# Performance work log

Measured on AMD Instinct MI355X. Metric: run time of the kernel, lower is better.

Reference implementation:

```python
import jax, jax.numpy as jnp
import numpy as np

N_HEAD, D_MODEL, D_K, D_V = 16, 1024, 64, 64
B, L = 8, 1024
LN_EPS = 1e-5
NEG_INF = -1e9


def setup_inputs() -> dict:
    key = jax.random.key(0)
    ks = jax.random.split(key, 12)
    s = 0.02
    return {
        "q": jax.random.normal(ks[0], (B, L, D_MODEL), jnp.float32),
        "k": jax.random.normal(ks[1], (B, L, D_MODEL), jnp.float32),
        "v": jax.random.normal(ks[2], (B, L, D_MODEL), jnp.float32),
        "mask": jnp.zeros((B, L, L), dtype=bool),
        "wq": jax.random.normal(ks[3], (D_MODEL, N_HEAD * D_K), jnp.float32) * s,
        "bq": jnp.zeros((N_HEAD * D_K,), jnp.float32),
        "wk": jax.random.normal(ks[4], (D_MODEL, N_HEAD * D_K), jnp.float32) * s,
        "bk": jnp.zeros((N_HEAD * D_K,), jnp.float32),
        "wv": jax.random.normal(ks[5], (D_MODEL, N_HEAD * D_V), jnp.float32) * s,
        "bv": jnp.zeros((N_HEAD * D_V,), jnp.float32),
        "wo": jax.random.normal(ks[6], (N_HEAD * D_V, D_MODEL), jnp.float32) * s,
        "bo": jnp.zeros((D_MODEL,), jnp.float32),
        "gamma": jnp.ones((D_MODEL,), jnp.float32),
        "beta": jnp.zeros((D_MODEL,), jnp.float32),
    }


def reference(q, k, v, mask, wq, bq, wk, bk, wv, bv, wo, bo, gamma, beta):
    b, lq, _ = q.shape
    lk = k.shape[1]
    residual = q
    # separate Q/K/V projections, split heads: [b, len, h, d]
    qh = (q @ wq + bq).reshape(b, lq, N_HEAD, D_K)
    kh = (k @ wk + bk).reshape(b, lk, N_HEAD, D_K)
    vh = (v @ wv + bv).reshape(b, lk, N_HEAD, D_V)
    # scaled dot-product attention (temperature = sqrt(d_k))
    scores = jnp.einsum("bqhd,bkhd->bhqk", qh, kh) / jnp.sqrt(jnp.float32(D_K))
    scores = jnp.where(mask[:, None, :, :], NEG_INF, scores)
    attn = jax.nn.softmax(scores, axis=-1)  # [b, h, lq, lk]
    ctx = jnp.einsum("bhqk,bkhd->bqhd", attn, vh).reshape(b, lq, N_HEAD * D_V)
    # out-proj (dropout is identity in eval) + residual + LayerNorm
    out = ctx @ wo + bo + residual
    mu = out.mean(-1, keepdims=True)
    var = out.var(-1, keepdims=True)
    out = (out - mu) * jax.lax.rsqrt(var + LN_EPS) * gamma + beta
    # match original attn layout: [n_head*b, lq, lk]
    attn_flat = attn.transpose(1, 0, 2, 3).reshape(N_HEAD * b, lq, lk)
    return out, attn_flat
```

## Files before the change

kernel.cpp:

```cpp
#include <hip/hip_runtime.h>
#include <stdint.h>

static constexpr int BATCH  = 8;
static constexpr int SEQ    = 1024;
static constexpr int DMODEL = 1024;
static constexpr int NHEAD  = 16;

typedef __attribute__((ext_vector_type(8))) short sh8;
typedef __attribute__((ext_vector_type(4))) float fl4;

__device__ __forceinline__ uint16_t f2bf(float f) {
    union { float f; uint32_t u; } a; a.f = f;
    uint32_t r = a.u + 0x7FFFu + ((a.u >> 16) & 1u);
    return (uint16_t)(r >> 16);
}

__device__ __forceinline__ float b2f(uint16_t u) {
    union { uint32_t u; float f; } a; a.u = ((uint32_t)u) << 16; return a.f;
}

__device__ __forceinline__ sh8 pack_bf8(fl4 x0, fl4 x1) {
    union { uint16_t u[8]; sh8 v; } pk;
    pk.u[0] = f2bf(x0[0]); pk.u[1] = f2bf(x0[1]); pk.u[2] = f2bf(x0[2]); pk.u[3] = f2bf(x0[3]);
    pk.u[4] = f2bf(x1[0]); pk.u[5] = f2bf(x1[1]); pk.u[6] = f2bf(x1[2]); pk.u[7] = f2bf(x1[3]);
    return pk.v;
}

__device__ __forceinline__ fl4 mfma16(sh8 a, sh8 b, fl4 c) {
    return __builtin_amdgcn_mfma_f32_16x16x32_bf16(a, b, c, 0, 0, 0);
}

__device__ __forceinline__ void gload16(const void* g, void* l) {
    __builtin_amdgcn_global_load_lds(
        (const __attribute__((address_space(1))) void*)g,
        (__attribute__((address_space(3))) void*)l, 16, 0, 0);
}

__global__ __launch_bounds__(256) void cvt_bf16_kernel(const float* __restrict__ src,
                                                       uint16_t* __restrict__ dst) {
    const int t = blockIdx.x * 256 + threadIdx.x;
    #pragma unroll
    for (int it = 0; it < 2; ++it) {
        const int i = (it * 524288 + t) * 8;
        fl4 x0 = *(const fl4*)(src + i), x1 = *(const fl4*)(src + i + 4);
        *(sh8*)(dst + i) = pack_bf8(x0, x1);
    }
}

__global__ __launch_bounds__(256) void wtrans_kernel(const float* __restrict__ w,
                                                     uint16_t* __restrict__ wT) {
    __shared__ uint16_t T[64][72];
    const int n0 = blockIdx.x * 64, k0 = blockIdx.y * 64;
    const int tid = threadIdx.x;
    #pragma unroll
    for (int it = 0; it < 4; ++it) {
        int g = it * 256 + tid;
        int r = g >> 4, c = (g & 15) * 4;
        fl4 x = *(const fl4*)(w + (size_t)(k0 + r) * DMODEL + n0 + c);
        T[r][c + 0] = f2bf(x[0]); T[r][c + 1] = f2bf(x[1]);
        T[r][c + 2] = f2bf(x[2]); T[r][c + 3] = f2bf(x[3]);
    }
    __syncthreads();
    #pragma unroll
    for (int it = 0; it < 4; ++it) {
        int g = it * 256 + tid;
        int r = g >> 4, c = (g & 15) * 4;
        ushort4 o;
        o.x = T[c + 0][r]; o.y = T[c + 1][r]; o.z = T[c + 2][r]; o.w = T[c + 3][r];
        *(ushort4*)(wT + (size_t)(n0 + r) * DMODEL + k0 + c) = o;
    }
}

__global__ __launch_bounds__(256) void vtrans_kernel(const uint16_t* __restrict__ vh,
                                                     uint16_t* __restrict__ vT) {
    __shared__ uint16_t T[64][72];
    const int l0 = blockIdx.x * 64, hd0 = blockIdx.y * 64, bb = blockIdx.z;
    const uint16_t* src = vh + (size_t)bb * SEQ * DMODEL;
    uint16_t* dst = vT + (size_t)bb * SEQ * DMODEL;
    const int tid = threadIdx.x;
    #pragma unroll
    for (int it = 0; it < 4; ++it) {
        int g = it * 256 + tid;
        int r = g >> 4, c = (g & 15) * 4;
        ushort4 x = *(const ushort4*)(src + (size_t)(l0 + r) * DMODEL + hd0 + c);
        T[r][c + 0] = x.x; T[r][c + 1] = x.y; T[r][c + 2] = x.z; T[r][c + 3] = x.w;
    }
    __syncthreads();
    #pragma unroll
    for (int it = 0; it < 4; ++it) {
        int g = it * 256 + tid;
        int r = g >> 4, c = (g & 15) * 4;
        ushort4 o;
        o.x = T[c + 0][r]; o.y = T[c + 1][r]; o.z = T[c + 2][r]; o.w = T[c + 3][r];
        *(ushort4*)(dst + (size_t)(hd0 + r) * DMODEL + l0 + c) = o;
    }
}

template<bool OUT_BF16, bool RESID>
__global__ __launch_bounds__(256)
void gemm128(const uint16_t* __restrict__ Ab, const uint16_t* __restrict__ Bt,
             const float* __restrict__ bias, const float* __restrict__ resid,
             void* __restrict__ Cv) {
    __shared__ uint16_t Alds[128 * 64];
    __shared__ uint16_t Blds[128 * 64];
    const int tid = threadIdx.x;
    const int m0 = blockIdx.y * 128, n0 = blockIdx.x * 128;
    const int lane = tid & 63, wid = tid >> 6;
    const int wr = (wid >> 1) * 64, wc = (wid & 1) * 64;
    const int fr = lane & 15, fk = (lane >> 4) * 8;

    fl4 acc[4][4];
    #pragma unroll
    for (int i = 0; i < 4; ++i)
        #pragma unroll
        for (int j = 0; j < 4; ++j) acc[i][j] = (fl4){0.f, 0.f, 0.f, 0.f};

    for (int kt = 0; kt < 16; ++kt) {
        const int kb = kt * 64;
        #pragma unroll
        for (int it = 0; it < 4; ++it) {
            const int g = it * 256 + tid;
            const int r = g >> 3, c = (g & 7) << 3;
            const int lofs = __builtin_amdgcn_readfirstlane((it * 256 + wid * 64) * 16);
            gload16(Ab + (size_t)(m0 + r) * DMODEL + kb + c, (char*)Alds + lofs);
            gload16(Bt + (size_t)(n0 + r) * DMODEL + kb + c, (char*)Blds + lofs);
        }
        __syncthreads();
        #pragma unroll
        for (int ks = 0; ks < 2; ++ks) {
            sh8 a[4], bb[4];
            #pragma unroll
            for (int mi = 0; mi < 4; ++mi) a[mi] = *(const sh8*)&Alds[(wr + mi * 16 + fr) * 64 + ks * 32 + fk];
            #pragma unroll
            for (int ni = 0; ni < 4; ++ni) bb[ni] = *(const sh8*)&Blds[(wc + ni * 16 + fr) * 64 + ks * 32 + fk];
            #pragma unroll
            for (int mi = 0; mi < 4; ++mi)
                #pragma unroll
                for (int ni = 0; ni < 4; ++ni) acc[mi][ni] = mfma16(a[mi], bb[ni], acc[mi][ni]);
        }
        __syncthreads();
    }

    #pragma unroll
    for (int mi = 0; mi < 4; ++mi) {
        #pragma unroll
        for (int ni = 0; ni < 4; ++ni) {
            const int col = n0 + wc + ni * 16 + fr;
            const float bv = bias[col];
            #pragma unroll
            for (int i = 0; i < 4; ++i) {
                const int row = m0 + wr + mi * 16 + (lane >> 4) * 4 + i;
                float val = acc[mi][ni][i] + bv;
                if (RESID) val += resid[(size_t)row * DMODEL + col];
                if (OUT_BF16) ((uint16_t*)Cv)[(size_t)row * DMODEL + col] = f2bf(val);
                else          ((float*)Cv)[(size_t)row * DMODEL + col] = val;
            }
        }
    }
}

__global__ __launch_bounds__(256)
void attn_kernel(const uint16_t* __restrict__ qh, const uint16_t* __restrict__ kh,
                 const uint16_t* __restrict__ vT, const uint8_t* __restrict__ mask,
                 float* __restrict__ attn, uint16_t* __restrict__ ctx) {
    __shared__ uint16_t S[16 * 1024];
    __shared__ float rinv[16];
    const int q0 = blockIdx.x * 16, h = blockIdx.y, b = blockIdx.z;
    const int tid = threadIdx.x, lane = tid & 63, wid = tid >> 6;
    const int fr = lane & 15, fk = (lane >> 4) * 8, frow4 = (lane >> 4) * 4;

    sh8 Aq[2];
    #pragma unroll
    for (int ks = 0; ks < 2; ++ks)
        Aq[ks] = *(const sh8*)(qh + (size_t)(b * SEQ + q0 + fr) * DMODEL + h * 64 + ks * 32 + fk);

    for (int t8 = 0; t8 < 8; ++t8) {
        const int kv0 = (t8 * 4 + wid) * 32;
        sh8 Bk[2][2];
        #pragma unroll
        for (int ni = 0; ni < 2; ++ni)
            #pragma unroll
            for (int ks = 0; ks < 2; ++ks)
                Bk[ni][ks] = *(const sh8*)(kh + (size_t)(b * SEQ + kv0 + ni * 16 + fr) * DMODEL + h * 64 + ks * 32 + fk);
        fl4 sa[2];
        #pragma unroll
        for (int ni = 0; ni < 2; ++ni) sa[ni] = (fl4){0.f, 0.f, 0.f, 0.f};
        #pragma unroll
        for (int ni = 0; ni < 2; ++ni)
            #pragma unroll
            for (int ks = 0; ks < 2; ++ks) sa[ni] = mfma16(Aq[ks], Bk[ni][ks], sa[ni]);
        #pragma unroll
        for (int ni = 0; ni < 2; ++ni)
            #pragma unroll
            for (int i = 0; i < 4; ++i) {
                const int row = frow4 + i, col = kv0 + ni * 16 + fr;
                S[row * 1024 + ((((col >> 3) ^ (row & 15)) << 3) | (col & 7))] = f2bf(sa[ni][i] * 0.125f);
            }
    }
    __syncthreads();

    {
        const int r = tid >> 4, j = tid & 15;
        const int rbase = r * 1024;
        const int rx = r & 15;
        const uint8_t* mbase = mask + (size_t)(b * SEQ + q0 + r) * SEQ;
        float mx = -1e30f;
        #pragma unroll
        for (int c4 = 0; c4 < 8; ++c4) {
            const int cc = c4 * 16 + j;
            const int so = rbase + ((cc ^ rx) << 3);
            sh8 sv = *(sh8*)&S[so];
            const uint2 mw = *(const uint2*)(mbase + cc * 8);
            union { uint16_t u[8]; sh8 v; } o;
            #pragma unroll
            for (int t = 0; t < 4; ++t) {
                float f = b2f((uint16_t)sv[t]);
                if ((mw.x >> (t * 8)) & 0xFF) f = -1e9f;
                o.u[t] = f2bf(f);
                mx = fmaxf(mx, f);
            }
            #pragma unroll
            for (int t = 0; t < 4; ++t) {
                float f = b2f((uint16_t)sv[4 + t]);
                if ((mw.y >> (t * 8)) & 0xFF) f = -1e9f;
                o.u[4 + t] = f2bf(f);
                mx = fmaxf(mx, f);
            }
            *(sh8*)&S[so] = o.v;
        }
        #pragma unroll
        for (int d = 1; d < 16; d <<= 1) mx = fmaxf(mx, __shfl_xor(mx, d));
        float sum = 0.f;
        #pragma unroll
        for (int c4 = 0; c4 < 8; ++c4) {
            const int cc = c4 * 16 + j;
            const int so = rbase + ((cc ^ rx) << 3);
            sh8 sv = *(sh8*)&S[so];
            union { uint16_t u[8]; sh8 v; } o;
            #pragma unroll
            for (int t = 0; t < 8; ++t) {
                float e = __expf(b2f((uint16_t)sv[t]) - mx);
                o.u[t] = f2bf(e);
                sum += e;
            }
            *(sh8*)&S[so] = o.v;
        }
        #pragma unroll
        for (int d = 1; d < 16; d <<= 1) sum += __shfl_xor(sum, d);
        if (j == 0) rinv[r] = 1.f / sum;
    }
    __syncthreads();

    {
        float* ab = attn + ((size_t)((h * BATCH + b) * SEQ + q0)) * SEQ;
        #pragma unroll
        for (int it = 0; it < 8; ++it) {
            const int gch = it * 256 + tid;
            const int row = gch >> 7, cc = gch & 127;
            sh8 p = *(sh8*)&S[row * 1024 + ((cc ^ (row & 15)) << 3)];
            const float ri = rinv[row];
            fl4 o0, o1;
            #pragma unroll
            for (int t = 0; t < 4; ++t) o0[t] = b2f((uint16_t)p[t]) * ri;
            #pragma unroll
            for (int t = 0; t < 4; ++t) o1[t] = b2f((uint16_t)p[4 + t]) * ri;
            float* dst = ab + (size_t)gch * 8;
            __builtin_nontemporal_store(o0, (fl4*)dst);
            __builtin_nontemporal_store(o1, (fl4*)(dst + 4));
        }
    }

    fl4 acc0 = (fl4){0.f, 0.f, 0.f, 0.f}, acc1 = (fl4){0.f, 0.f, 0.f, 0.f};
    const uint16_t* vbase = vT + (size_t)((b * NHEAD + h) * 64 + wid * 16) * SEQ;
    const int frx = fr & 15;
    #pragma unroll 4
    for (int ks2 = 0; ks2 < 32; ++ks2) {
        const int kv = ks2 * 32;
        sh8 Ap = *(const sh8*)&S[fr * 1024 + ((((kv + fk) >> 3) ^ frx) << 3)];
        sh8 Bv = *(const sh8*)(vbase + (size_t)fr * SEQ + kv + fk);
        if (ks2 & 1) acc1 = mfma16(Ap, Bv, acc1);
        else         acc0 = mfma16(Ap, Bv, acc0);
    }
    #pragma unroll
    for (int i = 0; i < 4; ++i) {
        const int q = frow4 + i;
        const float val = (acc0[i] + acc1[i]) * rinv[q];
        ctx[(size_t)(b * SEQ + q0 + q) * DMODEL + h * 64 + wid * 16 + fr] = f2bf(val);
    }
}

__global__ __launch_bounds__(256)
void ln_kernel(const float* __restrict__ raw, const float* __restrict__ gamma,
               const float* __restrict__ beta, float* __restrict__ out) {
    const int row = blockIdx.x;
    const int tid = threadIdx.x;
    const float* x = raw + (size_t)row * DMODEL;
    fl4 xv = *(const fl4*)(x + tid * 4);
    float s  = xv[0] + xv[1] + xv[2] + xv[3];
    float ss = xv[0] * xv[0] + xv[1] * xv[1] + xv[2] * xv[2] + xv[3] * xv[3];
    #pragma unroll
    for (int d = 1; d < 64; d <<= 1) { s += __shfl_xor(s, d); ss += __shfl_xor(ss, d); }
    __shared__ float sb[4], ssb[4];
    if ((tid & 63) == 0) { sb[tid >> 6] = s; ssb[tid >> 6] = ss; }
    __syncthreads();
    s  = sb[0] + sb[1] + sb[2] + sb[3];
    ss = ssb[0] + ssb[1] + ssb[2] + ssb[3];
    const float mu  = s * (1.f / 1024.f);
    const float var = ss * (1.f / 1024.f) - mu * mu;
    const float rstd = rsqrtf(var + 1e-5f);
    fl4 g  = *(const fl4*)(gamma + tid * 4);
    fl4 be = *(const fl4*)(beta + tid * 4);
    fl4 o;
    #pragma unroll
    for (int j = 0; j < 4; ++j) o[j] = (xv[j] - mu) * rstd * g[j] + be[j];
    *(fl4*)(out + (size_t)row * DMODEL + tid * 4) = o;
}

extern "C" void kernel_launch(void* const* d_in, const int* in_sizes, int n_in,
                              void* d_out, int out_size, void* d_ws, size_t ws_size,
                              hipStream_t stream) {
    (void)in_sizes; (void)n_in; (void)out_size; (void)ws_size;
    const float* q     = (const float*)d_in[0];
    const float* k     = (const float*)d_in[1];
    const float* v     = (const float*)d_in[2];
    const uint8_t* mask = (const uint8_t*)d_in[3];
    const float* wq = (const float*)d_in[4];
    const float* bq = (const float*)d_in[5];
    const float* wk = (const float*)d_in[6];
    const float* bk = (const float*)d_in[7];
    const float* wv = (const float*)d_in[8];
    const float* bv = (const float*)d_in[9];
    const float* wo = (const float*)d_in[10];
    const float* bo = (const float*)d_in[11];
    const float* gamma = (const float*)d_in[12];
    const float* beta  = (const float*)d_in[13];

    float* out  = (float*)d_out;
    float* attn = out + (size_t)BATCH * SEQ * DMODEL;

    uint16_t* qcvt = (uint16_t*)(attn);
    uint16_t* kcvt = (uint16_t*)((char*)attn + ((size_t)16 << 20));
    uint16_t* vcvt = (uint16_t*)((char*)attn + ((size_t)32 << 20));

    char* ws = (char*)d_ws;
    uint16_t* qh   = (uint16_t*)(ws);
    uint16_t* kh   = (uint16_t*)(ws + ((size_t)16 << 20));
    uint16_t* vT   = (uint16_t*)(ws + ((size_t)32 << 20));
    uint16_t* ctx  = (uint16_t*)(ws + ((size_t)48 << 20));
    uint16_t* wqT  = (uint16_t*)(ws + ((size_t)64 << 20));
    uint16_t* wkT  = (uint16_t*)(ws + ((size_t)66 << 20));
    uint16_t* wvT  = (uint16_t*)(ws + ((size_t)68 << 20));
    uint16_t* woT  = (uint16_t*)(ws + ((size_t)70 << 20));
    uint16_t* vtmp = (uint16_t*)(ws + ((size_t)72 << 20));

    dim3 tb(256);
    wtrans_kernel<<<dim3(16, 16), tb, 0, stream>>>(wq, wqT);
    wtrans_kernel<<<dim3(16, 16), tb, 0, stream>>>(wk, wkT);
    wtrans_kernel<<<dim3(16, 16), tb, 0, stream>>>(wv, wvT);
    wtrans_kernel<<<dim3(16, 16), tb, 0, stream>>>(wo, woT);

    cvt_bf16_kernel<<<2048, tb, 0, stream>>>(q, qcvt);
    cvt_bf16_kernel<<<2048, tb, 0, stream>>>(k, kcvt);
    cvt_bf16_kernel<<<2048, tb, 0, stream>>>(v, vcvt);

    gemm128<true, false><<<dim3(8, 64), tb, 0, stream>>>(qcvt, wqT, bq, nullptr, qh);
    gemm128<true, false><<<dim3(8, 64), tb, 0, stream>>>(kcvt, wkT, bk, nullptr, kh);
    gemm128<true, false><<<dim3(8, 64), tb, 0, stream>>>(vcvt, wvT, bv, nullptr, vtmp);

    vtrans_kernel<<<dim3(16, 16, 8), tb, 0, stream>>>(vtmp, vT);

    attn_kernel<<<dim3(64, NHEAD, BATCH), tb, 0, stream>>>(qh, kh, vT, mask, attn, ctx);

    gemm128<false, true><<<dim3(8, 64), tb, 0, stream>>>(ctx, woT, bo, q, out);

    ln_kernel<<<BATCH * SEQ, tb, 0, stream>>>(out, gamma, beta, out);
}
```

Baseline: 484.2 us.

## Batch weight transposes, conversions and QKV GEMMs; keep softmax row in registers

The four weight transposes, three fp32->bf16 conversions and three projection GEMMs are each merged into a single launch indexed by blockIdx.z. This cuts launch count and lets the three projection GEMMs fill the GPU together (1536 blocks instead of 512 per launch). The softmax now holds each thread's slice of the score row in registers, so it no longer re-reads shared memory between the max and exp passes. It also writes the fp32 attention output straight from registers instead of doing a separate synchronized pass over shared memory, at the cost of higher register pressure in the attention kernel.

```diff
diff --git a/kernel.cpp b/kernel.cpp
--- a/kernel.cpp
+++ b/kernel.cpp
@@ -36,8 +36,15 @@
         (__attribute__((address_space(3))) void*)l, 16, 0, 0);
 }
 
-__global__ __launch_bounds__(256) void cvt_bf16_kernel(const float* __restrict__ src,
-                                                       uint16_t* __restrict__ dst) {
+__global__ __launch_bounds__(256) void cvt3_kernel(const float* __restrict__ q,
+                                                   const float* __restrict__ k,
+                                                   const float* __restrict__ v,
+                                                   uint16_t* __restrict__ dq,
+                                                   uint16_t* __restrict__ dk,
+                                                   uint16_t* __restrict__ dv) {
+    const int z = blockIdx.z;
+    const float* src = (z == 0) ? q : (z == 1) ? k : v;
+    uint16_t* dst = (z == 0) ? dq : (z == 1) ? dk : dv;
     const int t = blockIdx.x * 256 + threadIdx.x;
     #pragma unroll
     for (int it = 0; it < 2; ++it) {
@@ -47,9 +54,14 @@
     }
 }
 
-__global__ __launch_bounds__(256) void wtrans_kernel(const float* __restrict__ w,
-                                                     uint16_t* __restrict__ wT) {
+__global__ __launch_bounds__(256) void wtrans_kernel(const float* __restrict__ wq, const float* __restrict__ wk,
+                                                     const float* __restrict__ wv, const float* __restrict__ wo,
+                                                     uint16_t* __restrict__ tq, uint16_t* __restrict__ tk,
+                                                     uint16_t* __restrict__ tv, uint16_t* __restrict__ to) {
     __shared__ uint16_t T[64][72];
+    const int z = blockIdx.z;
+    const float* w = (z == 0) ? wq : (z == 1) ? wk : (z == 2) ? wv : wo;
+    uint16_t* wT = (z == 0) ? tq : (z == 1) ? tk : (z == 2) ? tv : to;
     const int n0 = blockIdx.x * 64, k0 = blockIdx.y * 64;
     const int tid = threadIdx.x;
     #pragma unroll
@@ -97,14 +109,12 @@
 }
 
 template<bool OUT_BF16, bool RESID>
-__global__ __launch_bounds__(256)
-void gemm128(const uint16_t* __restrict__ Ab, const uint16_t* __restrict__ Bt,
-             const float* __restrict__ bias, const float* __restrict__ resid,
-             void* __restrict__ Cv) {
-    __shared__ uint16_t Alds[128 * 64];
-    __shared__ uint16_t Blds[128 * 64];
+__device__ __forceinline__
+void gemm_body(const uint16_t* __restrict__ Ab, const uint16_t* __restrict__ Bt,
+               const float* __restrict__ bias, const float* __restrict__ resid,
+               void* __restrict__ Cv, int m0, int n0,
+               uint16_t* Alds, uint16_t* Blds) {
     const int tid = threadIdx.x;
-    const int m0 = blockIdx.y * 128, n0 = blockIdx.x * 128;
     const int lane = tid & 63, wid = tid >> 6;
     const int wr = (wid >> 1) * 64, wc = (wid & 1) * 64;
     const int fr = lane & 15, fk = (lane >> 4) * 8;
@@ -157,6 +167,30 @@
             }
         }
     }
+}
+
+__global__ __launch_bounds__(256)
+void gemm_proj(const uint16_t* __restrict__ A0, const uint16_t* __restrict__ A1, const uint16_t* __restrict__ A2,
+               const uint16_t* __restrict__ B0, const uint16_t* __restrict__ B1, const uint16_t* __restrict__ B2,
+               const float* __restrict__ b0, const float* __restrict__ b1, const float* __restrict__ b2,
+               uint16_t* __restrict__ C0, uint16_t* __restrict__ C1, uint16_t* __restrict__ C2) {
+    __shared__ uint16_t Alds[128 * 64];
+    __shared__ uint16_t Blds[128 * 64];
+    const int z = blockIdx.z;
+    const uint16_t* Ab = (z == 0) ? A0 : (z == 1) ? A1 : A2;
+    const uint16_t* Bt = (z == 0) ? B0 : (z == 1) ? B1 : B2;
+    const float* bias  = (z == 0) ? b0 : (z == 1) ? b1 : b2;
+    uint16_t* Cv       = (z == 0) ? C0 : (z == 1) ? C1 : C2;
+    gemm_body<true, false>(Ab, Bt, bias, nullptr, Cv, blockIdx.y * 128, blockIdx.x * 128, Alds, Blds);
+}
+
+__global__ __launch_bounds__(256)
+void gemm_out(const uint16_t* __restrict__ Ab, const uint16_t* __restrict__ Bt,
+              const float* __restrict__ bias, const float* __restrict__ resid,
+              float* __restrict__ Cv) {
+    __shared__ uint16_t Alds[128 * 64];
+    __shared__ uint16_t Blds[128 * 64];
+    gemm_body<false, true>(Ab, Bt, bias, resid, Cv, blockIdx.y * 128, blockIdx.x * 128, Alds, Blds);
 }
 
 __global__ __launch_bounds__(256)
@@ -202,31 +236,30 @@
     {
         const int r = tid >> 4, j = tid & 15;
         const int rbase = r * 1024;
-        const int rx = r & 15;
         const uint8_t* mbase = mask + (size_t)(b * SEQ + q0 + r) * SEQ;
+        sh8 sv[8];
         float mx = -1e30f;
         #pragma unroll
         for (int c4 = 0; c4 < 8; ++c4) {
             const int cc = c4 * 16 + j;
-            const int so = rbase + ((cc ^ rx) << 3);
-            sh8 sv = *(sh8*)&S[so];
+            sh8 x = *(sh8*)&S[rbase + ((cc ^ r) << 3)];
             const uint2 mw = *(const uint2*)(mbase + cc * 8);
             union { uint16_t u[8]; sh8 v; } o;
             #pragma unroll
             for (int t = 0; t < 4; ++t) {
-                float f = b2f((uint16_t)sv[t]);
+                float f = b2f((uint16_t)x[t]);
                 if ((mw.x >> (t * 8)) & 0xFF) f = -1e9f;
                 o.u[t] = f2bf(f);
                 mx = fmaxf(mx, f);
             }
             #pragma unroll
             for (int t = 0; t < 4; ++t) {
-                float f = b2f((uint16_t)sv[4 + t]);
+                float f = b2f((uint16_t)x[4 + t]);
                 if ((mw.y >> (t * 8)) & 0xFF) f = -1e9f;
                 o.u[4 + t] = f2bf(f);
                 mx = fmaxf(mx, f);
             }
-            *(sh8*)&S[so] = o.v;
+            sv[c4] = o.v;
         }
         #pragma unroll
         for (int d = 1; d < 16; d <<= 1) mx = fmaxf(mx, __shfl_xor(mx, d));
@@ -234,41 +267,35 @@
         #pragma unroll
         for (int c4 = 0; c4 < 8; ++c4) {
             const int cc = c4 * 16 + j;
-            const int so = rbase + ((cc ^ rx) << 3);
-            sh8 sv = *(sh8*)&S[so];
             union { uint16_t u[8]; sh8 v; } o;
             #pragma unroll
             for (int t = 0; t < 8; ++t) {
-                float e = __expf(b2f((uint16_t)sv[t]) - mx);
+                float e = __expf(b2f((uint16_t)sv[c4][t]) - mx);
                 o.u[t] = f2bf(e);
                 sum += e;
             }
-            *(sh8*)&S[so] = o.v;
+            sv[c4] = o.v;
+            *(sh8*)&S[rbase + ((cc ^ r) << 3)] = o.v;
         }
         #pragma unroll
         for (int d = 1; d < 16; d <<= 1) sum += __shfl_xor(sum, d);
-        if (j == 0) rinv[r] = 1.f / sum;
-    }
-    __syncthreads();
-
-    {
-        float* ab = attn + ((size_t)((h * BATCH + b) * SEQ + q0)) * SEQ;
-        #pragma unroll
-        for (int it = 0; it < 8; ++it) {
-            const int gch = it * 256 + tid;
-            const int row = gch >> 7, cc = gch & 127;
-            sh8 p = *(sh8*)&S[row * 1024 + ((cc ^ (row & 15)) << 3)];
-            const float ri = rinv[row];
+        const float ri = 1.f / sum;
+        if (j == 0) rinv[r] = ri;
+        float* ab = attn + ((size_t)((h * BATCH + b) * SEQ + q0 + r)) * SEQ;
+        #pragma unroll
+        for (int c4 = 0; c4 < 8; ++c4) {
+            const int cc = c4 * 16 + j;
             fl4 o0, o1;
             #pragma unroll
-            for (int t = 0; t < 4; ++t) o0[t] = b2f((uint16_t)p[t]) * ri;
-            #pragma unroll
-            for (int t = 0; t < 4; ++t) o1[t] = b2f((uint16_t)p[4 + t]) * ri;
-            float* dst = ab + (size_t)gch * 8;
+            for (int t = 0; t < 4; ++t) o0[t] = b2f((uint16_t)sv[c4][t]) * ri;
+            #pragma unroll
+            for (int t = 0; t < 4; ++t) o1[t] = b2f((uint16_t)sv[c4][4 + t]) * ri;
+            float* dst = ab + cc * 8;
             __builtin_nontemporal_store(o0, (fl4*)dst);
             __builtin_nontemporal_store(o1, (fl4*)(dst + 4));
         }
     }
+    __syncthreads();
 
     fl4 acc0 = (fl4){0.f, 0.f, 0.f, 0.f}, acc1 = (fl4){0.f, 0.f, 0.f, 0.f};
     const uint16_t* vbase = vT + (size_t)((b * NHEAD + h) * 64 + wid * 16) * SEQ;
@@ -354,24 +381,17 @@
     uint16_t* vtmp = (uint16_t*)(ws + ((size_t)72 << 20));
 
     dim3 tb(256);
-    wtrans_kernel<<<dim3(16, 16), tb, 0, stream>>>(wq, wqT);
-    wtrans_kernel<<<dim3(16, 16), tb, 0, stream>>>(wk, wkT);
-    wtrans_kernel<<<dim3(16, 16), tb, 0, stream>>>(wv, wvT);
-    wtrans_kernel<<<dim3(16, 16), tb, 0, stream>>>(wo, woT);
-
-    cvt_bf16_kernel<<<2048, tb, 0, stream>>>(q, qcvt);
-    cvt_bf16_kernel<<<2048, tb, 0, stream>>>(k, kcvt);
-    cvt_bf16_kernel<<<2048, tb, 0, stream>>>(v, vcvt);
-
-    gemm128<true, false><<<dim3(8, 64), tb, 0, stream>>>(qcvt, wqT, bq, nullptr, qh);
-    gemm128<true, false><<<dim3(8, 64), tb, 0, stream>>>(kcvt, wkT, bk, nullptr, kh);
-    gemm128<true, false><<<dim3(8, 64), tb, 0, stream>>>(vcvt, wvT, bv, nullptr, vtmp);
+    wtrans_kernel<<<dim3(16, 16, 4), tb, 0, stream>>>(wq, wk, wv, wo, wqT, wkT, wvT, woT);
+    cvt3_kernel<<<dim3(2048, 1, 3), tb, 0, stream>>>(q, k, v, qcvt, kcvt, vcvt);
+
+    gemm_proj<<<dim3(8, 64, 3), tb, 0, stream>>>(qcvt, kcvt, vcvt, wqT, wkT, wvT,
+                                                 bq, bk, bv, qh, kh, vtmp);
 
     vtrans_kernel<<<dim3(16, 16, 8), tb, 0, stream>>>(vtmp, vT);
 
     attn_kernel<<<dim3(64, NHEAD, BATCH), tb, 0, stream>>>(qh, kh, vT, mask, attn, ctx);
 
-    gemm128<false, true><<<dim3(8, 64), tb, 0, stream>>>(ctx, woT, bo, q, out);
+    gemm_out<<<dim3(8, 64), tb, 0, stream>>>(ctx, woT, bo, q, out);
 
     ln_kernel<<<BATCH * SEQ, tb, 0, stream>>>(out, gamma, beta, out);
 }
```

Result: faster. 456.4 us (-5.7%).
